# Performance work log

Hardware: AMD Instinct MI355X
Metric: run time of the kernel (lower is better)

## Reference

```python
import jax, jax.numpy as jnp
import numpy as np

IN_CH, OUT_CH, HIDDEN_FREQ, M1, M2 = 32, 32, 64, 32, 32
B, H, W = 8, 256, 256


def setup_inputs() -> dict:
    key = jax.random.key(0)
    k1, k2, k3, k4, k5 = jax.random.split(key, 5)
    scale = 1.0 / (IN_CH * OUT_CH)
    x = jax.random.normal(k1, (B, IN_CH, H, W), dtype=jnp.float32)
    mod1 = jax.random.normal(k2, (B, 1, 1, M1, M2, 2), dtype=jnp.float32)
    mod2 = jax.random.normal(k3, (B, 1, 1, M1, M2, 2), dtype=jnp.float32)
    weights = scale * jax.random.uniform(k4, (IN_CH, OUT_CH, 2, HIDDEN_FREQ), dtype=jnp.float32)
    # torch Linear(hidden_freq, m1*m2*2, bias=False): weight (m1*m2*2, hidden_freq)
    lim = 1.0 / np.sqrt(HIDDEN_FREQ)
    mlp_w = jax.random.uniform(k5, (M1 * M2 * 2, HIDDEN_FREQ), dtype=jnp.float32, minval=-lim, maxval=lim)
    return {"x": x, "mod1": mod1, "mod2": mod2, "weights": weights, "mlp_w": mlp_w}


def reference(x, mod1, mod2, weights, mlp_w):
    Bn, Ci, Hn, Wn = x.shape
    Co = weights.shape[1]
    x_ft = jnp.fft.rfft2(x)  # (B, Ci, H, W//2+1) complex
    # MLP-generated spectral weights: (Ci, Co, 2, hidden) @ (hidden, m1*m2*2)
    w = (weights @ mlp_w.T).reshape(Ci, Co, 2, M1, M2, 2)
    wc = jax.lax.complex(w[..., 0], w[..., 1])        # (Ci, Co, 2, M1, M2)
    mod1c = jax.lax.complex(mod1[..., 0], mod1[..., 1])  # (B,1,1,M1,M2)
    mod2c = jax.lax.complex(mod2[..., 0], mod2[..., 1])
    cm1 = wc[:, :, 0] * mod1c  # (B, Ci, Co, M1, M2)
    cm2 = wc[:, :, 1] * mod2c
    out1 = jnp.einsum('bixy,bioxy->boxy', x_ft[:, :, :M1, :M2], cm1)
    out2 = jnp.einsum('bixy,bioxy->boxy', x_ft[:, :, -M1:, :M2], cm2)
    out_ft = jnp.zeros((Bn, Co, Hn, Wn // 2 + 1), dtype=x_ft.dtype)
    out_ft = out_ft.at[:, :, :M1, :M2].set(out1)
    out_ft = out_ft.at[:, :, -M1:, :M2].set(out2)
    return jnp.fft.irfft2(out_ft, s=(Hn, Wn))
```

## Files before the change

kernel.cpp:

```cpp
#include <hip/hip_runtime.h>

#define BB 8
#define CI 32
#define CO 32
#define HH 256
#define WW 256
#define HF 64
#define KX 32
#define NJ 64

typedef __attribute__((ext_vector_type(8))) short short8;
typedef __attribute__((ext_vector_type(4))) float f32x4;

__device__ __constant__ float PI2 = 6.28318530717958647692f;

#define PK_E   0
#define PK_D   32768
#define PK_TF  65536
#define PK_A2  131072
#define PK_TOTAL 196608

__device__ inline unsigned short f2bf(float f) {
    unsigned u = __float_as_uint(f);
    u += 0x7FFF + ((u >> 16) & 1);
    return (unsigned short)(u >> 16);
}
__device__ inline void splitbf(float f, unsigned short& h, unsigned short& l) {
    unsigned short hh = f2bf(f);
    float fh = __uint_as_float(((unsigned)hh) << 16);
    l = f2bf(f - fh);
    h = hh;
}

__global__ void kprep(unsigned short* __restrict__ pk) {
    int id = blockIdx.x * 256 + threadIdx.x;
    if (id < 16384) {
        int j = id & 7, lane = (id >> 3) & 63, nt = (id >> 9) & 3, kt = id >> 11;
        int k = kt * 32 + (lane >> 4) * 8 + j;
        int n = nt * 16 + (lane & 15);
        int kx = n >> 1, c = n & 1;
        int p = (k * kx) & 255;
        float sn, cs; sincosf(PI2 * (float)p / 256.0f, &sn, &cs);
        float val = c ? -sn : cs;
        unsigned short h, l; splitbf(val, h, l);
        pk[id] = h; pk[id + 16384] = l;
    } else if (id < 32768) {
        int id2 = id - 16384;
        int j = id2 & 7, lane = (id2 >> 3) & 63, nt = (id2 >> 9) & 15, kt = id2 >> 13;
        int k = kt * 32 + (lane >> 4) * 8 + j;
        int w = nt * 16 + (lane & 15);
        int kx = k >> 1, c = k & 1;
        int p = (kx * w) & 255;
        float sn, cs; sincosf(PI2 * (float)p / 256.0f, &sn, &cs);
        float ck = (kx == 0) ? 1.0f : 2.0f;
        float val = c ? -ck * sn : ck * cs;
        unsigned short h, l; splitbf(val, h, l);
        pk[PK_D + id2] = h; pk[PK_D + 16384 + id2] = l;
    } else if (id < 65536) {
        int idt = id - 32768;
        int e = idt & 7, lane = (idt >> 3) & 63, kt = (idt >> 9) & 7, mt = (idt >> 12) & 3, p = (idt >> 14) & 1;
        int j = mt * 16 + (lane & 15);
        int h = kt * 32 + (lane >> 4) * 8 + e;
        int ky = (j < 32) ? j : (192 + j);
        int ang = (ky * h) & 255;
        float sn, cs; sincosf(PI2 * (float)ang / 256.0f, &sn, &cs);
        float val = p ? sn : cs;
        unsigned short hh, ll; splitbf(val, hh, ll);
        int base = PK_TF + p * 32768 + mt * 4096 + kt * 512 + lane * 8 + e;
        pk[base] = hh; pk[base + 16384] = ll;
    } else {
        int ida = id - 65536;
        int e = ida & 7, lane = (ida >> 3) & 63, kt = (ida >> 9) & 3, mt = ida >> 11;
        int h = mt * 16 + (lane & 15);
        int kp = kt * 32 + (lane >> 4) * 8 + e;
        int j = kp & 63, p = kp >> 6;
        int ky = (j < 32) ? j : (192 + j);
        int ang = (ky * h) & 255;
        float sn, cs; sincosf(PI2 * (float)ang / 256.0f, &sn, &cs);
        float val = p ? sn : cs;
        unsigned short hh, ll; splitbf(val, hh, ll);
        pk[PK_A2 + ida] = hh; pk[PK_A2 + 32768 + ida] = ll;
    }
}

__global__ __launch_bounds__(256) void kweights(const float* __restrict__ wts,
                                                const float* __restrict__ mlp,
                                                float* __restrict__ WC) {
    int t = threadIdx.x;
    int wid = t >> 6, lane = t & 63;
    int bm = blockIdx.x >> 4, bn = blockIdx.x & 15;
    int m0 = bm * 128 + (wid >> 1) * 64;
    int n0 = bn * 128 + (wid & 1) * 64;
    int l15 = lane & 15, lq = lane >> 4;

    f32x4 acc[4][4];
    #pragma unroll
    for (int mt = 0; mt < 4; mt++)
        #pragma unroll
        for (int nt = 0; nt < 4; nt++)
            acc[mt][nt] = (f32x4){0.f, 0.f, 0.f, 0.f};

    #pragma unroll
    for (int kt = 0; kt < 2; kt++) {
        short8 Ah[4], Al[4];
        #pragma unroll
        for (int mt = 0; mt < 4; mt++) {
            int m = m0 + mt * 16 + l15;
            int c = m >> 10, mm = m & 1023;
            const float4* p = (const float4*)(mlp + (mm * 2 + c) * 64 + kt * 32 + lq * 8);
            float4 v0 = p[0], v1 = p[1];
            float vals[8] = {v0.x, v0.y, v0.z, v0.w, v1.x, v1.y, v1.z, v1.w};
            #pragma unroll
            for (int e = 0; e < 8; e++) {
                unsigned short h, l; splitbf(vals[e], h, l);
                Ah[mt][e] = (short)h; Al[mt][e] = (short)l;
            }
        }
        #pragma unroll
        for (int nt = 0; nt < 4; nt++) {
            int n = n0 + nt * 16 + l15;
            int s = n >> 10, io = n & 1023;
            const float4* p = (const float4*)(wts + (io * 2 + s) * 64 + kt * 32 + lq * 8);
            float4 v0 = p[0], v1 = p[1];
            float vals[8] = {v0.x, v0.y, v0.z, v0.w, v1.x, v1.y, v1.z, v1.w};
            short8 Bh, Bl;
            #pragma unroll
            for (int e = 0; e < 8; e++) {
                unsigned short h, l; splitbf(vals[e], h, l);
                Bh[e] = (short)h; Bl[e] = (short)l;
            }
            #pragma unroll
            for (int mt = 0; mt < 4; mt++) {
                acc[mt][nt] = __builtin_amdgcn_mfma_f32_16x16x32_bf16(Ah[mt], Bh, acc[mt][nt], 0, 0, 0);
                acc[mt][nt] = __builtin_amdgcn_mfma_f32_16x16x32_bf16(Ah[mt], Bl, acc[mt][nt], 0, 0, 0);
                acc[mt][nt] = __builtin_amdgcn_mfma_f32_16x16x32_bf16(Al[mt], Bh, acc[mt][nt], 0, 0, 0);
            }
        }
    }
    #pragma unroll
    for (int mt = 0; mt < 4; mt++)
        #pragma unroll
        for (int nt = 0; nt < 4; nt++)
            #pragma unroll
            for (int r = 0; r < 4; r++) {
                int m = m0 + mt * 16 + lq * 4 + r;
                int n = n0 + nt * 16 + l15;
                int addr = (((n >> 10) * 1024 + (m & 1023)) * 2 + (m >> 10)) * 1024 + (n & 1023);
                WC[addr] = acc[mt][nt][r];
            }
}

#define XS_STR 264
__global__ __launch_bounds__(512) void kfwd(const float* __restrict__ x,
                                            const unsigned short* __restrict__ pk,
                                            float* __restrict__ F) {
    __shared__ short Xbf[2][64 * XS_STR];
    int t = threadIdx.x;
    int bi = blockIdx.x;
    int w = t >> 6, lane = t & 63;
    int l15 = lane & 15, lq = lane >> 4;

    f32x4 acc[2][4];
    #pragma unroll
    for (int mt = 0; mt < 2; mt++)
        #pragma unroll
        for (int nt = 0; nt < 4; nt++)
            acc[mt][nt] = (f32x4){0.f, 0.f, 0.f, 0.f};

    #pragma unroll
    for (int kt = 0; kt < 8; kt++) {
        short8 bh[4], bl[4];
        #pragma unroll
        for (int nt = 0; nt < 4; nt++) {
            bh[nt] = *(const short8*)(pk + ((size_t)((kt * 4 + nt) * 64 + lane)) * 8);
            bl[nt] = *(const short8*)(pk + 16384 + ((size_t)((kt * 4 + nt) * 64 + lane)) * 8);
        }
        #pragma unroll
        for (int mt = 0; mt < 2; mt++) {
            const float4* ap = (const float4*)(x + (size_t)(bi * 256 + w * 32 + mt * 16 + l15) * 256 + kt * 32 + lq * 8);
            float4 v0 = ap[0], v1 = ap[1];
            float vals[8] = {v0.x, v0.y, v0.z, v0.w, v1.x, v1.y, v1.z, v1.w};
            short8 ah, al;
            #pragma unroll
            for (int e = 0; e < 8; e++) {
                unsigned short h, l; splitbf(vals[e], h, l);
                ah[e] = (short)h; al[e] = (short)l;
            }
            #pragma unroll
            for (int nt = 0; nt < 4; nt++) {
                acc[mt][nt] = __builtin_amdgcn_mfma_f32_16x16x32_bf16(ah, bh[nt], acc[mt][nt], 0, 0, 0);
                acc[mt][nt] = __builtin_amdgcn_mfma_f32_16x16x32_bf16(ah, bl[nt], acc[mt][nt], 0, 0, 0);
                acc[mt][nt] = __builtin_amdgcn_mfma_f32_16x16x32_bf16(al, bh[nt], acc[mt][nt], 0, 0, 0);
            }
        }
    }
    #pragma unroll
    for (int mt = 0; mt < 2; mt++)
        #pragma unroll
        for (int nt = 0; nt < 4; nt++)
            #pragma unroll
            for (int r = 0; r < 4; r++) {
                int hrow = w * 32 + mt * 16 + lq * 4 + r;
                int n = nt * 16 + l15;
                unsigned short hh, ll; splitbf(acc[mt][nt][r], hh, ll);
                Xbf[0][n * XS_STR + hrow] = (short)hh;
                Xbf[1][n * XS_STR + hrow] = (short)ll;
            }
    __syncthreads();

    int mtq = w >> 1, ntbase = (w & 1) * 2;
    f32x4 ca[2], cb[2];
    ca[0] = (f32x4){0.f,0.f,0.f,0.f}; ca[1] = (f32x4){0.f,0.f,0.f,0.f};
    cb[0] = (f32x4){0.f,0.f,0.f,0.f}; cb[1] = (f32x4){0.f,0.f,0.f,0.f};
    #pragma unroll
    for (int kt = 0; kt < 8; kt++) {
        int aoff = PK_TF + mtq * 4096 + kt * 512 + lane * 8;
        short8 Ach = *(const short8*)(pk + aoff);
        short8 Acl = *(const short8*)(pk + aoff + 16384);
        short8 Ash = *(const short8*)(pk + aoff + 32768);
        short8 Asl = *(const short8*)(pk + aoff + 49152);
        #pragma unroll
        for (int ntl = 0; ntl < 2; ntl++) {
            int n = (ntbase + ntl) * 16 + l15;
            short8 xh = *(const short8*)&Xbf[0][n * XS_STR + kt * 32 + lq * 8];
            short8 xl = *(const short8*)&Xbf[1][n * XS_STR + kt * 32 + lq * 8];
            ca[ntl] = __builtin_amdgcn_mfma_f32_16x16x32_bf16(Ach, xh, ca[ntl], 0, 0, 0);
            ca[ntl] = __builtin_amdgcn_mfma_f32_16x16x32_bf16(Ach, xl, ca[ntl], 0, 0, 0);
            ca[ntl] = __builtin_amdgcn_mfma_f32_16x16x32_bf16(Acl, xh, ca[ntl], 0, 0, 0);
            cb[ntl] = __builtin_amdgcn_mfma_f32_16x16x32_bf16(Ash, xh, cb[ntl], 0, 0, 0);
            cb[ntl] = __builtin_amdgcn_mfma_f32_16x16x32_bf16(Ash, xl, cb[ntl], 0, 0, 0);
            cb[ntl] = __builtin_amdgcn_mfma_f32_16x16x32_bf16(Asl, xh, cb[ntl], 0, 0, 0);
        }
    }
    #pragma unroll
    for (int ntl = 0; ntl < 2; ntl++) {
        int n = (ntbase + ntl) * 16 + l15;
        #pragma unroll
        for (int r = 0; r < 4; r++) {
            float a = ca[ntl][r];
            float bsw = __shfl_xor(cb[ntl][r], 1, 64);
            float out = (n & 1) ? (a - bsw) : (a + bsw);
            int j = mtq * 16 + lq * 4 + r;
            F[(size_t)bi * 4096 + j * 64 + n] = out;
        }
    }
}

__global__ void kmodes(const float* __restrict__ F, const float* __restrict__ WC,
                       const float* __restrict__ mod1, const float* __restrict__ mod2,
                       float* __restrict__ OM) {
    int m = blockIdx.x;
    int j = m >> 5, kx = m & 31;
    int s = j >> 5;
    int m1 = j & 31, m2 = kx;
    __shared__ float2 fs[BB][CI];
    __shared__ float wcr[CI * CO];
    __shared__ float wci[CI * CO];
    int t = threadIdx.x;
    {
        int b = t >> 5, i = t & 31;
        fs[b][i] = ((const float2*)F)[((size_t)(b * CI + i) * NJ + j) * KX + kx];
    }
    {
        const float4* wg = (const float4*)(WC + ((size_t)(s * 1024 + m1 * 32 + m2) * 2) * 1024);
        ((float4*)wcr)[t] = wg[t];
        ((float4*)wci)[t] = wg[t + 256];
    }
    __syncthreads();
    int b = t >> 5, o = t & 31;
    float ar = 0.f, ai = 0.f;
    #pragma unroll 8
    for (int i = 0; i < CI; i++) {
        float2 f = fs[b][i];
        float wx = wcr[i * 32 + o];
        float wy = wci[i * 32 + o];
        ar = fmaf(f.x, wx, ar);
        ar = fmaf(-f.y, wy, ar);
        ai = fmaf(f.x, wy, ai);
        ai = fmaf(f.y, wx, ai);
    }
    const float* mp = (s == 0) ? mod1 : mod2;
    float mr = mp[(b * 1024 + m1 * 32 + m2) * 2 + 0];
    float mi = mp[(b * 1024 + m1 * 32 + m2) * 2 + 1];
    const float scale = 1.0f / 65536.0f;
    float outr = (ar * mr - ai * mi) * scale;
    float outi = (ar * mi + ai * mr) * scale;
    ((float2*)OM)[((size_t)(b * CO + o) * NJ + j) * KX + kx] = make_float2(outr, outi);
}

#define BP_STR 136
#define GB_STR 72
__global__ __launch_bounds__(512) void kinv(const float* __restrict__ OM,
                                            const unsigned short* __restrict__ pk,
                                            float* __restrict__ y) {
    __shared__ short smem[2 * 256 * GB_STR];
    short* Bp0 = smem;
    short* Bp1 = smem + 64 * BP_STR;
    short* G0 = smem;
    short* G1 = smem + 256 * GB_STR;
    int t = threadIdx.x;
    int bo = blockIdx.x;
    int lane = t & 63, w = t >> 6;
    int l15 = lane & 15, lq = lane >> 4;

    {
        const float4* src = (const float4*)OM + (size_t)bo * 1024;
        #pragma unroll
        for (int q = 0; q < 2; q++) {
            int idx4 = t + q * 512;
            float4 v = src[idx4];
            #pragma unroll
            for (int half = 0; half < 2; half++) {
                int e = idx4 * 2 + half;
                int j = e >> 5, kx = e & 31;
                float Or = half ? v.z : v.x;
                float Oi = half ? v.w : v.y;
                unsigned short orh, orl, oih, oil, nih, nil;
                splitbf(Or, orh, orl);
                splitbf(Oi, oih, oil);
                splitbf(-Oi, nih, nil);
                Bp0[(2 * kx) * BP_STR + j] = (short)orh;      Bp1[(2 * kx) * BP_STR + j] = (short)orl;
                Bp0[(2 * kx) * BP_STR + 64 + j] = (short)nih; Bp1[(2 * kx) * BP_STR + 64 + j] = (short)nil;
                Bp0[(2 * kx + 1) * BP_STR + j] = (short)oih;  Bp1[(2 * kx + 1) * BP_STR + j] = (short)oil;
                Bp0[(2 * kx + 1) * BP_STR + 64 + j] = (short)orh; Bp1[(2 * kx + 1) * BP_STR + 64 + j] = (short)orl;
            }
        }
    }
    __syncthreads();

    f32x4 g[2][4];
    #pragma unroll
    for (int mtl = 0; mtl < 2; mtl++)
        #pragma unroll
        for (int nt = 0; nt < 4; nt++)
            g[mtl][nt] = (f32x4){0.f, 0.f, 0.f, 0.f};
    #pragma unroll
    for (int kt = 0; kt < 4; kt++) {
        short8 a2h[2], a2l[2];
        #pragma unroll
        for (int mtl = 0; mtl < 2; mtl++) {
            int mt = w * 2 + mtl;
            int aoff = PK_A2 + mt * 2048 + kt * 512 + lane * 8;
            a2h[mtl] = *(const short8*)(pk + aoff);
            a2l[mtl] = *(const short8*)(pk + aoff + 32768);
        }
        #pragma unroll
        for (int nt = 0; nt < 4; nt++) {
            int n = nt * 16 + l15;
            short8 bh = *(const short8*)&Bp0[n * BP_STR + kt * 32 + lq * 8];
            short8 bl = *(const short8*)&Bp1[n * BP_STR + kt * 32 + lq * 8];
            #pragma unroll
            for (int mtl = 0; mtl < 2; mtl++) {
                g[mtl][nt] = __builtin_amdgcn_mfma_f32_16x16x32_bf16(a2h[mtl], bh, g[mtl][nt], 0, 0, 0);
                g[mtl][nt] = __builtin_amdgcn_mfma_f32_16x16x32_bf16(a2h[mtl], bl, g[mtl][nt], 0, 0, 0);
                g[mtl][nt] = __builtin_amdgcn_mfma_f32_16x16x32_bf16(a2l[mtl], bh, g[mtl][nt], 0, 0, 0);
            }
        }
    }
    __syncthreads();

    #pragma unroll
    for (int mtl = 0; mtl < 2; mtl++)
        #pragma unroll
        for (int nt = 0; nt < 4; nt++)
            #pragma unroll
            for (int r = 0; r < 4; r++) {
                int h = (w * 2 + mtl) * 16 + lq * 4 + r;
                int n = nt * 16 + l15;
                unsigned short hh, ll; splitbf(g[mtl][nt][r], hh, ll);
                G0[h * GB_STR + n] = (short)hh;
                G1[h * GB_STR + n] = (short)ll;
            }
    __syncthreads();

    const unsigned short* pkD = pk + PK_D;
    short8 Bh[2][2], Bl[2][2];
    #pragma unroll
    for (int kt = 0; kt < 2; kt++)
        #pragma unroll
        for (int ntl = 0; ntl < 2; ntl++) {
            int nt = w * 2 + ntl;
            Bh[kt][ntl] = *(const short8*)(pkD + ((size_t)((kt * 16 + nt) * 64 + lane)) * 8);
            Bl[kt][ntl] = *(const short8*)(pkD + 16384 + ((size_t)((kt * 16 + nt) * 64 + lane)) * 8);
        }
    #pragma unroll 4
    for (int mt = 0; mt < 16; mt++) {
        f32x4 acc2[2];
        acc2[0] = (f32x4){0.f, 0.f, 0.f, 0.f};
        acc2[1] = (f32x4){0.f, 0.f, 0.f, 0.f};
        #pragma unroll
        for (int kt = 0; kt < 2; kt++) {
            short8 ah = *(const short8*)&G0[(mt * 16 + l15) * GB_STR + kt * 32 + lq * 8];
            short8 al = *(const short8*)&G1[(mt * 16 + l15) * GB_STR + kt * 32 + lq * 8];
            #pragma unroll
            for (int ntl = 0; ntl < 2; ntl++) {
                acc2[ntl] = __builtin_amdgcn_mfma_f32_16x16x32_bf16(ah, Bh[kt][ntl], acc2[ntl], 0, 0, 0);
                acc2[ntl] = __builtin_amdgcn_mfma_f32_16x16x32_bf16(ah, Bl[kt][ntl], acc2[ntl], 0, 0, 0);
                acc2[ntl] = __builtin_amdgcn_mfma_f32_16x16x32_bf16(al, Bh[kt][ntl], acc2[ntl], 0, 0, 0);
            }
        }
        #pragma unroll
        for (int ntl = 0; ntl < 2; ntl++)
            #pragma unroll
            for (int r = 0; r < 4; r++)
                y[(size_t)(bo * 256 + mt * 16 + lq * 4 + r) * 256 + (w * 2 + ntl) * 16 + l15] = acc2[ntl][r];
    }
}

extern "C" void kernel_launch(void* const* d_in, const int* in_sizes, int n_in,
                              void* d_out, int out_size, void* d_ws, size_t ws_size,
                              hipStream_t stream) {
    const float* x    = (const float*)d_in[0];
    const float* mod1 = (const float*)d_in[1];
    const float* mod2 = (const float*)d_in[2];
    const float* wts  = (const float*)d_in[3];
    const float* mlp  = (const float*)d_in[4];
    float* y = (float*)d_out;

    float* ws = (float*)d_ws;
    float* F  = ws;
    float* WC = F + 1048576;
    float* OM = WC + 4194304;
    unsigned short* pk = (unsigned short*)(OM + 1048576);

    kprep   <<<dim3(384),  dim3(256), 0, stream>>>(pk);
    kweights<<<dim3(256),  dim3(256), 0, stream>>>(wts, mlp, WC);
    kfwd    <<<dim3(BB * CI), dim3(512), 0, stream>>>(x, pk, F);
    kmodes  <<<dim3(NJ * KX), dim3(256), 0, stream>>>(F, WC, mod1, mod2, OM);
    kinv    <<<dim3(BB * CO), dim3(512), 0, stream>>>(OM, pk, y);
}
```

Before: 167.9 us.

## Switch split-precision MFMA to fp16, merge prep kernels, stage x via async LDS loads

Replaces the bf16 hi/lo split with an fp16 hi/lo split, using fp16 MFMA and adding scaling factors to keep values in fp16 range. The twiddle-prep and weight-generation kernels are merged into one launch. The forward kernel now double-buffers x tiles into shared memory with global_load_lds under a swizzled layout, overlapping loads with MFMA work. The 1/65536 normalization moves from the mode kernel to the final output. These changes target launch overhead, global-load latency in the forward DFT and bit-manipulation cost, but fp16's narrow exponent range risks overflow or underflow.

```diff
diff --git a/kernel.cpp b/kernel.cpp
--- a/kernel.cpp
+++ b/kernel.cpp
@@ -9,7 +9,7 @@
 #define KX 32
 #define NJ 64
 
-typedef __attribute__((ext_vector_type(8))) short short8;
+typedef __attribute__((ext_vector_type(8))) _Float16 half8;
 typedef __attribute__((ext_vector_type(4))) float f32x4;
 
 __device__ __constant__ float PI2 = 6.28318530717958647692f;
@@ -18,77 +18,72 @@
 #define PK_D   32768
 #define PK_TF  65536
 #define PK_A2  131072
-#define PK_TOTAL 196608
-
-__device__ inline unsigned short f2bf(float f) {
-    unsigned u = __float_as_uint(f);
-    u += 0x7FFF + ((u >> 16) & 1);
-    return (unsigned short)(u >> 16);
-}
-__device__ inline void splitbf(float f, unsigned short& h, unsigned short& l) {
-    unsigned short hh = f2bf(f);
-    float fh = __uint_as_float(((unsigned)hh) << 16);
-    l = f2bf(f - fh);
-    h = hh;
-}
-
-__global__ void kprep(unsigned short* __restrict__ pk) {
-    int id = blockIdx.x * 256 + threadIdx.x;
-    if (id < 16384) {
-        int j = id & 7, lane = (id >> 3) & 63, nt = (id >> 9) & 3, kt = id >> 11;
-        int k = kt * 32 + (lane >> 4) * 8 + j;
-        int n = nt * 16 + (lane & 15);
-        int kx = n >> 1, c = n & 1;
-        int p = (k * kx) & 255;
-        float sn, cs; sincosf(PI2 * (float)p / 256.0f, &sn, &cs);
-        float val = c ? -sn : cs;
-        unsigned short h, l; splitbf(val, h, l);
-        pk[id] = h; pk[id + 16384] = l;
-    } else if (id < 32768) {
-        int id2 = id - 16384;
-        int j = id2 & 7, lane = (id2 >> 3) & 63, nt = (id2 >> 9) & 15, kt = id2 >> 13;
-        int k = kt * 32 + (lane >> 4) * 8 + j;
-        int w = nt * 16 + (lane & 15);
-        int kx = k >> 1, c = k & 1;
-        int p = (kx * w) & 255;
-        float sn, cs; sincosf(PI2 * (float)p / 256.0f, &sn, &cs);
-        float ck = (kx == 0) ? 1.0f : 2.0f;
-        float val = c ? -ck * sn : ck * cs;
-        unsigned short h, l; splitbf(val, h, l);
-        pk[PK_D + id2] = h; pk[PK_D + 16384 + id2] = l;
-    } else if (id < 65536) {
-        int idt = id - 32768;
-        int e = idt & 7, lane = (idt >> 3) & 63, kt = (idt >> 9) & 7, mt = (idt >> 12) & 3, p = (idt >> 14) & 1;
-        int j = mt * 16 + (lane & 15);
-        int h = kt * 32 + (lane >> 4) * 8 + e;
-        int ky = (j < 32) ? j : (192 + j);
-        int ang = (ky * h) & 255;
-        float sn, cs; sincosf(PI2 * (float)ang / 256.0f, &sn, &cs);
-        float val = p ? sn : cs;
-        unsigned short hh, ll; splitbf(val, hh, ll);
-        int base = PK_TF + p * 32768 + mt * 4096 + kt * 512 + lane * 8 + e;
-        pk[base] = hh; pk[base + 16384] = ll;
-    } else {
-        int ida = id - 65536;
-        int e = ida & 7, lane = (ida >> 3) & 63, kt = (ida >> 9) & 3, mt = ida >> 11;
-        int h = mt * 16 + (lane & 15);
-        int kp = kt * 32 + (lane >> 4) * 8 + e;
-        int j = kp & 63, p = kp >> 6;
-        int ky = (j < 32) ? j : (192 + j);
-        int ang = (ky * h) & 255;
-        float sn, cs; sincosf(PI2 * (float)ang / 256.0f, &sn, &cs);
-        float val = p ? sn : cs;
-        unsigned short hh, ll; splitbf(val, hh, ll);
-        pk[PK_A2 + ida] = hh; pk[PK_A2 + 32768 + ida] = ll;
-    }
-}
-
-__global__ __launch_bounds__(256) void kweights(const float* __restrict__ wts,
-                                                const float* __restrict__ mlp,
-                                                float* __restrict__ WC) {
+
+__device__ inline void splitf16(float f, _Float16& h, _Float16& l) {
+    h = (_Float16)f;
+    l = (_Float16)(f - (float)h);
+}
+
+__global__ __launch_bounds__(256) void kprepw(const float* __restrict__ wts,
+                                              const float* __restrict__ mlp,
+                                              float* __restrict__ WC,
+                                              _Float16* __restrict__ pk) {
+    if (blockIdx.x < 384) {
+        int id = blockIdx.x * 256 + threadIdx.x;
+        if (id < 16384) {
+            int j = id & 7, lane = (id >> 3) & 63, nt = (id >> 9) & 3, kt = id >> 11;
+            int k = kt * 32 + (lane >> 4) * 8 + j;
+            int n = nt * 16 + (lane & 15);
+            int kx = n >> 1, c = n & 1;
+            int p = (k * kx) & 255;
+            float sn, cs; sincosf(PI2 * (float)p / 256.0f, &sn, &cs);
+            float val = c ? -sn : cs;
+            _Float16 h, l; splitf16(val, h, l);
+            pk[id] = h; pk[id + 16384] = l;
+        } else if (id < 32768) {
+            int id2 = id - 16384;
+            int j = id2 & 7, lane = (id2 >> 3) & 63, nt = (id2 >> 9) & 15, kt = id2 >> 13;
+            int k = kt * 32 + (lane >> 4) * 8 + j;
+            int w = nt * 16 + (lane & 15);
+            int kx = k >> 1, c = k & 1;
+            int p = (kx * w) & 255;
+            float sn, cs; sincosf(PI2 * (float)p / 256.0f, &sn, &cs);
+            float ck = (kx == 0) ? 1.0f : 2.0f;
+            float val = c ? -ck * sn : ck * cs;
+            _Float16 h, l; splitf16(val, h, l);
+            pk[PK_D + id2] = h; pk[PK_D + 16384 + id2] = l;
+        } else if (id < 65536) {
+            int idt = id - 32768;
+            int e = idt & 7, lane = (idt >> 3) & 63, kt = (idt >> 9) & 7, mt = (idt >> 12) & 3, p = (idt >> 14) & 1;
+            int j = mt * 16 + (lane & 15);
+            int h = kt * 32 + (lane >> 4) * 8 + e;
+            int ky = (j < 32) ? j : (192 + j);
+            int ang = (ky * h) & 255;
+            float sn, cs; sincosf(PI2 * (float)ang / 256.0f, &sn, &cs);
+            float val = p ? sn : cs;
+            _Float16 hh, ll; splitf16(val, hh, ll);
+            int base = PK_TF + p * 32768 + mt * 4096 + kt * 512 + lane * 8 + e;
+            pk[base] = hh; pk[base + 16384] = ll;
+        } else {
+            int ida = id - 65536;
+            int e = ida & 7, lane = (ida >> 3) & 63, kt = (ida >> 9) & 3, mt = ida >> 11;
+            int h = mt * 16 + (lane & 15);
+            int kp = kt * 32 + (lane >> 4) * 8 + e;
+            int j = kp & 63, p = kp >> 6;
+            int ky = (j < 32) ? j : (192 + j);
+            int ang = (ky * h) & 255;
+            float sn, cs; sincosf(PI2 * (float)ang / 256.0f, &sn, &cs);
+            float val = p ? sn : cs;
+            _Float16 hh, ll; splitf16(val, hh, ll);
+            pk[PK_A2 + ida] = hh; pk[PK_A2 + 32768 + ida] = ll;
+        }
+        return;
+    }
+
     int t = threadIdx.x;
     int wid = t >> 6, lane = t & 63;
-    int bm = blockIdx.x >> 4, bn = blockIdx.x & 15;
+    int bid = blockIdx.x - 384;
+    int bm = bid >> 4, bn = bid & 15;
     int m0 = bm * 128 + (wid >> 1) * 64;
     int n0 = bn * 128 + (wid & 1) * 64;
     int l15 = lane & 15, lq = lane >> 4;
@@ -102,7 +97,7 @@
 
     #pragma unroll
     for (int kt = 0; kt < 2; kt++) {
-        short8 Ah[4], Al[4];
+        half8 Ah[4], Al[4];
         #pragma unroll
         for (int mt = 0; mt < 4; mt++) {
             int m = m0 + mt * 16 + l15;
@@ -112,8 +107,8 @@
             float vals[8] = {v0.x, v0.y, v0.z, v0.w, v1.x, v1.y, v1.z, v1.w};
             #pragma unroll
             for (int e = 0; e < 8; e++) {
-                unsigned short h, l; splitbf(vals[e], h, l);
-                Ah[mt][e] = (short)h; Al[mt][e] = (short)l;
+                _Float16 h, l; splitf16(vals[e] * 8.0f, h, l);
+                Ah[mt][e] = h; Al[mt][e] = l;
             }
         }
         #pragma unroll
@@ -123,17 +118,17 @@
             const float4* p = (const float4*)(wts + (io * 2 + s) * 64 + kt * 32 + lq * 8);
             float4 v0 = p[0], v1 = p[1];
             float vals[8] = {v0.x, v0.y, v0.z, v0.w, v1.x, v1.y, v1.z, v1.w};
-            short8 Bh, Bl;
+            half8 Bh, Bl;
             #pragma unroll
             for (int e = 0; e < 8; e++) {
-                unsigned short h, l; splitbf(vals[e], h, l);
-                Bh[e] = (short)h; Bl[e] = (short)l;
+                _Float16 h, l; splitf16(vals[e] * 4096.0f, h, l);
+                Bh[e] = h; Bl[e] = l;
             }
             #pragma unroll
             for (int mt = 0; mt < 4; mt++) {
-                acc[mt][nt] = __builtin_amdgcn_mfma_f32_16x16x32_bf16(Ah[mt], Bh, acc[mt][nt], 0, 0, 0);
-                acc[mt][nt] = __builtin_amdgcn_mfma_f32_16x16x32_bf16(Ah[mt], Bl, acc[mt][nt], 0, 0, 0);
-                acc[mt][nt] = __builtin_amdgcn_mfma_f32_16x16x32_bf16(Al[mt], Bh, acc[mt][nt], 0, 0, 0);
+                acc[mt][nt] = __builtin_amdgcn_mfma_f32_16x16x32_f16(Ah[mt], Bh, acc[mt][nt], 0, 0, 0);
+                acc[mt][nt] = __builtin_amdgcn_mfma_f32_16x16x32_f16(Ah[mt], Bl, acc[mt][nt], 0, 0, 0);
+                acc[mt][nt] = __builtin_amdgcn_mfma_f32_16x16x32_f16(Al[mt], Bh, acc[mt][nt], 0, 0, 0);
             }
         }
     }
@@ -146,19 +141,35 @@
                 int m = m0 + mt * 16 + lq * 4 + r;
                 int n = n0 + nt * 16 + l15;
                 int addr = (((n >> 10) * 1024 + (m & 1023)) * 2 + (m >> 10)) * 1024 + (n & 1023);
-                WC[addr] = acc[mt][nt][r];
+                WC[addr] = acc[mt][nt][r] * (1.0f / 32768.0f);
             }
 }
 
 #define XS_STR 264
 __global__ __launch_bounds__(512) void kfwd(const float* __restrict__ x,
-                                            const unsigned short* __restrict__ pk,
+                                            const _Float16* __restrict__ pk,
                                             float* __restrict__ F) {
-    __shared__ short Xbf[2][64 * XS_STR];
+    __shared__ float xs[2][8192];
+    __shared__ _Float16 Xbf[2][64 * XS_STR];
     int t = threadIdx.x;
     int bi = blockIdx.x;
     int w = t >> 6, lane = t & 63;
     int l15 = lane & 15, lq = lane >> 4;
+    const float* xsl = x + ((size_t)bi << 16);
+
+#define STAGE(ktt, sel) do {                                                   \
+    _Pragma("unroll")                                                          \
+    for (int i_ = 0; i_ < 4; i_++) {                                           \
+        int c_ = i_ * 512 + w * 64 + lane;                                     \
+        int row_ = c_ >> 3;                                                    \
+        int gs_ = (c_ & 7) ^ (row_ & 7);                                       \
+        const float* gp_ = xsl + row_ * 256 + (ktt) * 32 + gs_ * 4;            \
+        __builtin_amdgcn_global_load_lds(                                      \
+            (const __attribute__((address_space(1))) unsigned int*)gp_,        \
+            (__attribute__((address_space(3))) unsigned int*)&xs[sel][(i_ * 512 + w * 64) * 4], \
+            16, 0, 0);                                                         \
+    }                                                                          \
+} while (0)
 
     f32x4 acc[2][4];
     #pragma unroll
@@ -167,33 +178,47 @@
         for (int nt = 0; nt < 4; nt++)
             acc[mt][nt] = (f32x4){0.f, 0.f, 0.f, 0.f};
 
-    #pragma unroll
+    STAGE(0, 0);
     for (int kt = 0; kt < 8; kt++) {
-        short8 bh[4], bl[4];
+        int sel = kt & 1;
+        half8 Eh[4], El[4];
         #pragma unroll
         for (int nt = 0; nt < 4; nt++) {
-            bh[nt] = *(const short8*)(pk + ((size_t)((kt * 4 + nt) * 64 + lane)) * 8);
-            bl[nt] = *(const short8*)(pk + 16384 + ((size_t)((kt * 4 + nt) * 64 + lane)) * 8);
-        }
+            Eh[nt] = *(const half8*)(pk + ((size_t)((kt * 4 + nt) * 64 + lane)) * 8);
+            El[nt] = *(const half8*)(pk + 16384 + ((size_t)((kt * 4 + nt) * 64 + lane)) * 8);
+        }
+        if (kt < 7) {
+            STAGE(kt + 1, sel ^ 1);
+            asm volatile("s_waitcnt vmcnt(4)" ::: "memory");
+        } else {
+            asm volatile("s_waitcnt vmcnt(0)" ::: "memory");
+        }
+        __builtin_amdgcn_s_barrier();
         #pragma unroll
         for (int mt = 0; mt < 2; mt++) {
-            const float4* ap = (const float4*)(x + (size_t)(bi * 256 + w * 32 + mt * 16 + l15) * 256 + kt * 32 + lq * 8);
-            float4 v0 = ap[0], v1 = ap[1];
-            float vals[8] = {v0.x, v0.y, v0.z, v0.w, v1.x, v1.y, v1.z, v1.w};
-            short8 ah, al;
+            int row = w * 32 + mt * 16 + l15;
+            int g0 = (2 * lq) ^ (row & 7);
+            float4 va = *(const float4*)&xs[sel][row * 32 + g0 * 4];
+            float4 vb = *(const float4*)&xs[sel][row * 32 + (g0 ^ 1) * 4];
+            float vals[8] = {va.x, va.y, va.z, va.w, vb.x, vb.y, vb.z, vb.w};
+            half8 ah, al;
             #pragma unroll
             for (int e = 0; e < 8; e++) {
-                unsigned short h, l; splitbf(vals[e], h, l);
-                ah[e] = (short)h; al[e] = (short)l;
+                _Float16 h, l; splitf16(vals[e], h, l);
+                ah[e] = h; al[e] = l;
             }
             #pragma unroll
             for (int nt = 0; nt < 4; nt++) {
-                acc[mt][nt] = __builtin_amdgcn_mfma_f32_16x16x32_bf16(ah, bh[nt], acc[mt][nt], 0, 0, 0);
-                acc[mt][nt] = __builtin_amdgcn_mfma_f32_16x16x32_bf16(ah, bl[nt], acc[mt][nt], 0, 0, 0);
-                acc[mt][nt] = __builtin_amdgcn_mfma_f32_16x16x32_bf16(al, bh[nt], acc[mt][nt], 0, 0, 0);
-            }
-        }
-    }
+                acc[mt][nt] = __builtin_amdgcn_mfma_f32_16x16x32_f16(ah, Eh[nt], acc[mt][nt], 0, 0, 0);
+                acc[mt][nt] = __builtin_amdgcn_mfma_f32_16x16x32_f16(ah, El[nt], acc[mt][nt], 0, 0, 0);
+                acc[mt][nt] = __builtin_amdgcn_mfma_f32_16x16x32_f16(al, Eh[nt], acc[mt][nt], 0, 0, 0);
+            }
+        }
+        asm volatile("s_waitcnt lgkmcnt(0)" ::: "memory");
+        __builtin_amdgcn_s_barrier();
+    }
+#undef STAGE
+
     #pragma unroll
     for (int mt = 0; mt < 2; mt++)
         #pragma unroll
@@ -202,9 +227,9 @@
             for (int r = 0; r < 4; r++) {
                 int hrow = w * 32 + mt * 16 + lq * 4 + r;
                 int n = nt * 16 + l15;
-                unsigned short hh, ll; splitbf(acc[mt][nt][r], hh, ll);
-                Xbf[0][n * XS_STR + hrow] = (short)hh;
-                Xbf[1][n * XS_STR + hrow] = (short)ll;
+                _Float16 hh, ll; splitf16(acc[mt][nt][r], hh, ll);
+                Xbf[0][n * XS_STR + hrow] = hh;
+                Xbf[1][n * XS_STR + hrow] = ll;
             }
     __syncthreads();
 
@@ -215,21 +240,21 @@
     #pragma unroll
     for (int kt = 0; kt < 8; kt++) {
         int aoff = PK_TF + mtq * 4096 + kt * 512 + lane * 8;
-        short8 Ach = *(const short8*)(pk + aoff);
-        short8 Acl = *(const short8*)(pk + aoff + 16384);
-        short8 Ash = *(const short8*)(pk + aoff + 32768);
-        short8 Asl = *(const short8*)(pk + aoff + 49152);
+        half8 Ach = *(const half8*)(pk + aoff);
+        half8 Acl = *(const half8*)(pk + aoff + 16384);
+        half8 Ash = *(const half8*)(pk + aoff + 32768);
+        half8 Asl = *(const half8*)(pk + aoff + 49152);
         #pragma unroll
         for (int ntl = 0; ntl < 2; ntl++) {
             int n = (ntbase + ntl) * 16 + l15;
-            short8 xh = *(const short8*)&Xbf[0][n * XS_STR + kt * 32 + lq * 8];
-            short8 xl = *(const short8*)&Xbf[1][n * XS_STR + kt * 32 + lq * 8];
-            ca[ntl] = __builtin_amdgcn_mfma_f32_16x16x32_bf16(Ach, xh, ca[ntl], 0, 0, 0);
-            ca[ntl] = __builtin_amdgcn_mfma_f32_16x16x32_bf16(Ach, xl, ca[ntl], 0, 0, 0);
-            ca[ntl] = __builtin_amdgcn_mfma_f32_16x16x32_bf16(Acl, xh, ca[ntl], 0, 0, 0);
-            cb[ntl] = __builtin_amdgcn_mfma_f32_16x16x32_bf16(Ash, xh, cb[ntl], 0, 0, 0);
-            cb[ntl] = __builtin_amdgcn_mfma_f32_16x16x32_bf16(Ash, xl, cb[ntl], 0, 0, 0);
-            cb[ntl] = __builtin_amdgcn_mfma_f32_16x16x32_bf16(Asl, xh, cb[ntl], 0, 0, 0);
+            half8 xh = *(const half8*)&Xbf[0][n * XS_STR + kt * 32 + lq * 8];
+            half8 xl = *(const half8*)&Xbf[1][n * XS_STR + kt * 32 + lq * 8];
+            ca[ntl] = __builtin_amdgcn_mfma_f32_16x16x32_f16(Ach, xh, ca[ntl], 0, 0, 0);
+            ca[ntl] = __builtin_amdgcn_mfma_f32_16x16x32_f16(Ach, xl, ca[ntl], 0, 0, 0);
+            ca[ntl] = __builtin_amdgcn_mfma_f32_16x16x32_f16(Acl, xh, ca[ntl], 0, 0, 0);
+            cb[ntl] = __builtin_amdgcn_mfma_f32_16x16x32_f16(Ash, xh, cb[ntl], 0, 0, 0);
+            cb[ntl] = __builtin_amdgcn_mfma_f32_16x16x32_f16(Ash, xl, cb[ntl], 0, 0, 0);
+            cb[ntl] = __builtin_amdgcn_mfma_f32_16x16x32_f16(Asl, xh, cb[ntl], 0, 0, 0);
         }
     }
     #pragma unroll
@@ -282,22 +307,21 @@
     const float* mp = (s == 0) ? mod1 : mod2;
     float mr = mp[(b * 1024 + m1 * 32 + m2) * 2 + 0];
     float mi = mp[(b * 1024 + m1 * 32 + m2) * 2 + 1];
-    const float scale = 1.0f / 65536.0f;
-    float outr = (ar * mr - ai * mi) * scale;
-    float outi = (ar * mi + ai * mr) * scale;
+    float outr = (ar * mr - ai * mi);
+    float outi = (ar * mi + ai * mr);
     ((float2*)OM)[((size_t)(b * CO + o) * NJ + j) * KX + kx] = make_float2(outr, outi);
 }
 
 #define BP_STR 136
 #define GB_STR 72
 __global__ __launch_bounds__(512) void kinv(const float* __restrict__ OM,
-                                            const unsigned short* __restrict__ pk,
+                                            const _Float16* __restrict__ pk,
                                             float* __restrict__ y) {
-    __shared__ short smem[2 * 256 * GB_STR];
-    short* Bp0 = smem;
-    short* Bp1 = smem + 64 * BP_STR;
-    short* G0 = smem;
-    short* G1 = smem + 256 * GB_STR;
+    __shared__ _Float16 smem[2 * 256 * GB_STR];
+    _Float16* Bp0 = smem;
+    _Float16* Bp1 = smem + 64 * BP_STR;
+    _Float16* G0 = smem;
+    _Float16* G1 = smem + 256 * GB_STR;
     int t = threadIdx.x;
     int bo = blockIdx.x;
     int lane = t & 63, w = t >> 6;
@@ -315,14 +339,13 @@
                 int j = e >> 5, kx = e & 31;
                 float Or = half ? v.z : v.x;
                 float Oi = half ? v.w : v.y;
-                unsigned short orh, orl, oih, oil, nih, nil;
-                splitbf(Or, orh, orl);
-                splitbf(Oi, oih, oil);
-                splitbf(-Oi, nih, nil);
-                Bp0[(2 * kx) * BP_STR + j] = (short)orh;      Bp1[(2 * kx) * BP_STR + j] = (short)orl;
-                Bp0[(2 * kx) * BP_STR + 64 + j] = (short)nih; Bp1[(2 * kx) * BP_STR + 64 + j] = (short)nil;
-                Bp0[(2 * kx + 1) * BP_STR + j] = (short)oih;  Bp1[(2 * kx + 1) * BP_STR + j] = (short)oil;
-                Bp0[(2 * kx + 1) * BP_STR + 64 + j] = (short)orh; Bp1[(2 * kx + 1) * BP_STR + 64 + j] = (short)orl;
+                _Float16 orh, orl, oih, oil;
+                splitf16(Or, orh, orl);
+                splitf16(Oi, oih, oil);
+                Bp0[(2 * kx) * BP_STR + j] = orh;           Bp1[(2 * kx) * BP_STR + j] = orl;
+                Bp0[(2 * kx) * BP_STR + 64 + j] = -oih;     Bp1[(2 * kx) * BP_STR + 64 + j] = -oil;
+                Bp0[(2 * kx + 1) * BP_STR + j] = oih;       Bp1[(2 * kx + 1) * BP_STR + j] = oil;
+                Bp0[(2 * kx + 1) * BP_STR + 64 + j] = orh;  Bp1[(2 * kx + 1) * BP_STR + 64 + j] = orl;
             }
         }
     }
@@ -336,24 +359,24 @@
             g[mtl][nt] = (f32x4){0.f, 0.f, 0.f, 0.f};
     #pragma unroll
     for (int kt = 0; kt < 4; kt++) {
-        short8 a2h[2], a2l[2];
+        half8 a2h[2], a2l[2];
         #pragma unroll
         for (int mtl = 0; mtl < 2; mtl++) {
             int mt = w * 2 + mtl;
             int aoff = PK_A2 + mt * 2048 + kt * 512 + lane * 8;
-            a2h[mtl] = *(const short8*)(pk + aoff);
-            a2l[mtl] = *(const short8*)(pk + aoff + 32768);
+            a2h[mtl] = *(const half8*)(pk + aoff);
+            a2l[mtl] = *(const half8*)(pk + aoff + 32768);
         }
         #pragma unroll
         for (int nt = 0; nt < 4; nt++) {
             int n = nt * 16 + l15;
-            short8 bh = *(const short8*)&Bp0[n * BP_STR + kt * 32 + lq * 8];
-            short8 bl = *(const short8*)&Bp1[n * BP_STR + kt * 32 + lq * 8];
+            half8 bh = *(const half8*)&Bp0[n * BP_STR + kt * 32 + lq * 8];
+            half8 bl = *(const half8*)&Bp1[n * BP_STR + kt * 32 + lq * 8];
             #pragma unroll
             for (int mtl = 0; mtl < 2; mtl++) {
-                g[mtl][nt] = __builtin_amdgcn_mfma_f32_16x16x32_bf16(a2h[mtl], bh, g[mtl][nt], 0, 0, 0);
-                g[mtl][nt] = __builtin_amdgcn_mfma_f32_16x16x32_bf16(a2h[mtl], bl, g[mtl][nt], 0, 0, 0);
-                g[mtl][nt] = __builtin_amdgcn_mfma_f32_16x16x32_bf16(a2l[mtl], bh, g[mtl][nt], 0, 0, 0);
+                g[mtl][nt] = __builtin_amdgcn_mfma_f32_16x16x32_f16(a2h[mtl], bh, g[mtl][nt], 0, 0, 0);
+                g[mtl][nt] = __builtin_amdgcn_mfma_f32_16x16x32_f16(a2h[mtl], bl, g[mtl][nt], 0, 0, 0);
+                g[mtl][nt] = __builtin_amdgcn_mfma_f32_16x16x32_f16(a2l[mtl], bh, g[mtl][nt], 0, 0, 0);
             }
         }
     }
@@ -367,21 +390,21 @@
             for (int r = 0; r < 4; r++) {
                 int h = (w * 2 + mtl) * 16 + lq * 4 + r;
                 int n = nt * 16 + l15;
-                unsigned short hh, ll; splitbf(g[mtl][nt][r], hh, ll);
-                G0[h * GB_STR + n] = (short)hh;
-                G1[h * GB_STR + n] = (short)ll;
+                _Float16 hh, ll; splitf16(g[mtl][nt][r], hh, ll);
+                G0[h * GB_STR + n] = hh;
+                G1[h * GB_STR + n] = ll;
             }
     __syncthreads();
 
-    const unsigned short* pkD = pk + PK_D;
-    short8 Bh[2][2], Bl[2][2];
+    const _Float16* pkD = pk + PK_D;
+    half8 Bh[2][2], Bl[2][2];
     #pragma unroll
     for (int kt = 0; kt < 2; kt++)
         #pragma unroll
         for (int ntl = 0; ntl < 2; ntl++) {
             int nt = w * 2 + ntl;
-            Bh[kt][ntl] = *(const short8*)(pkD + ((size_t)((kt * 16 + nt) * 64 + lane)) * 8);
-            Bl[kt][ntl] = *(const short8*)(pkD + 16384 + ((size_t)((kt * 16 + nt) * 64 + lane)) * 8);
+            Bh[kt][ntl] = *(const half8*)(pkD + ((size_t)((kt * 16 + nt) * 64 + lane)) * 8);
+            Bl[kt][ntl] = *(const half8*)(pkD + 16384 + ((size_t)((kt * 16 + nt) * 64 + lane)) * 8);
         }
     #pragma unroll 4
     for (int mt = 0; mt < 16; mt++) {
@@ -390,20 +413,21 @@
         acc2[1] = (f32x4){0.f, 0.f, 0.f, 0.f};
         #pragma unroll
         for (int kt = 0; kt < 2; kt++) {
-            short8 ah = *(const short8*)&G0[(mt * 16 + l15) * GB_STR + kt * 32 + lq * 8];
-            short8 al = *(const short8*)&G1[(mt * 16 + l15) * GB_STR + kt * 32 + lq * 8];
+            half8 ah = *(const half8*)&G0[(mt * 16 + l15) * GB_STR + kt * 32 + lq * 8];
+            half8 al = *(const half8*)&G1[(mt * 16 + l15) * GB_STR + kt * 32 + lq * 8];
             #pragma unroll
             for (int ntl = 0; ntl < 2; ntl++) {
-                acc2[ntl] = __builtin_amdgcn_mfma_f32_16x16x32_bf16(ah, Bh[kt][ntl], acc2[ntl], 0, 0, 0);
-                acc2[ntl] = __builtin_amdgcn_mfma_f32_16x16x32_bf16(ah, Bl[kt][ntl], acc2[ntl], 0, 0, 0);
-                acc2[ntl] = __builtin_amdgcn_mfma_f32_16x16x32_bf16(al, Bh[kt][ntl], acc2[ntl], 0, 0, 0);
+                acc2[ntl] = __builtin_amdgcn_mfma_f32_16x16x32_f16(ah, Bh[kt][ntl], acc2[ntl], 0, 0, 0);
+                acc2[ntl] = __builtin_amdgcn_mfma_f32_16x16x32_f16(ah, Bl[kt][ntl], acc2[ntl], 0, 0, 0);
+                acc2[ntl] = __builtin_amdgcn_mfma_f32_16x16x32_f16(al, Bh[kt][ntl], acc2[ntl], 0, 0, 0);
             }
         }
         #pragma unroll
         for (int ntl = 0; ntl < 2; ntl++)
             #pragma unroll
             for (int r = 0; r < 4; r++)
-                y[(size_t)(bo * 256 + mt * 16 + lq * 4 + r) * 256 + (w * 2 + ntl) * 16 + l15] = acc2[ntl][r];
+                y[(size_t)(bo * 256 + mt * 16 + lq * 4 + r) * 256 + (w * 2 + ntl) * 16 + l15] =
+                    acc2[ntl][r] * (1.0f / 65536.0f);
     }
 }
 
@@ -421,11 +445,10 @@
     float* F  = ws;
     float* WC = F + 1048576;
     float* OM = WC + 4194304;
-    unsigned short* pk = (unsigned short*)(OM + 1048576);
-
-    kprep   <<<dim3(384),  dim3(256), 0, stream>>>(pk);
-    kweights<<<dim3(256),  dim3(256), 0, stream>>>(wts, mlp, WC);
-    kfwd    <<<dim3(BB * CI), dim3(512), 0, stream>>>(x, pk, F);
-    kmodes  <<<dim3(NJ * KX), dim3(256), 0, stream>>>(F, WC, mod1, mod2, OM);
-    kinv    <<<dim3(BB * CO), dim3(512), 0, stream>>>(OM, pk, y);
-}
+    _Float16* pk = (_Float16*)(OM + 1048576);
+
+    kprepw<<<dim3(640),  dim3(256), 0, stream>>>(wts, mlp, WC, pk);
+    kfwd  <<<dim3(BB * CI), dim3(512), 0, stream>>>(x, pk, F);
+    kmodes<<<dim3(NJ * KX), dim3(256), 0, stream>>>(F, WC, mod1, mod2, OM);
+    kinv  <<<dim3(BB * CO), dim3(512), 0, stream>>>(OM, pk, y);
+}
```

Measured after the change: 164.7 us. About the same (-1.9%).
